# Performance work log

Measured on AMD Instinct MI355X. Metric: run time of the kernel, lower is better.

## Reference

```python
import jax, jax.numpy as jnp
import numpy as np

N_NODES = 100000
N_EDGES = 1600000
HIDDEN = 64
LEAKY_SLOPE = 0.01  # torch F.leaky_relu default


def setup_inputs() -> dict:
    key = jax.random.key(0)
    k1, k2, k3, k4 = jax.random.split(key, 4)
    x = jax.random.normal(k1, (N_NODES, HIDDEN), dtype=jnp.float32)
    edge_index = jax.random.randint(k2, (2, N_EDGES), 0, N_NODES, dtype=jnp.int64)
    # Linear(hidden, 1, bias=False) weights, squeezed to [hidden]
    w_i = jax.random.normal(k3, (HIDDEN,), dtype=jnp.float32) * 0.1
    w_j = jax.random.normal(k4, (HIDDEN,), dtype=jnp.float32) * 0.1
    return {"x": x, "edge_index": edge_index, "w_i": w_i, "w_j": w_j}


def reference(x, edge_index, w_i, w_j):
    n = x.shape[0]
    ej, ei = edge_index[0], edge_index[1]  # (edge_index_j, edge_index_i)
    # per-node attention scores, then per-edge gather
    s_i = x @ w_i  # [N]
    s_j = x @ w_j  # [N]
    e = jax.nn.leaky_relu(s_i[ei] + s_j[ej], LEAKY_SLOPE)  # [E]
    # segment softmax over edges grouped by destination node ei
    emax = jax.ops.segment_max(e, ei, num_segments=n)  # [N]
    ex = jnp.exp(e - emax[ei])  # [E]
    denom = jax.ops.segment_sum(ex, ei, num_segments=n)  # [N]
    alpha = ex / denom[ei]  # [E]
    # spmm: out[i] = sum_{edges e: dst=i} alpha_e * x[src_e]
    out = jax.ops.segment_sum(alpha[:, None] * x[ej], ei, num_segments=n)  # [N, H]
    return jax.nn.relu(out)
```

## Files before the change

kernel.cpp:

```cpp
#include <hip/hip_runtime.h>
#include <stdint.h>

#define N_NODES 100000
#define N_EDGES 1600000
#define HIDDEN  64
#define SLOPE   0.01f
#define NBUCK   782
#define CAPB    2816
#define PCHUNK  16384
#define NPART   98
#define NSB     391
#define NCAP    48


__device__ __forceinline__ unsigned short f2bf(float f) {
    uint32_t u = __float_as_uint(f);
    uint32_t r = u + 0x7FFFu + ((u >> 16) & 1u);
    return (unsigned short)(r >> 16);
}

__global__ void __launch_bounds__(1024) k_build(const float* __restrict__ x,
                                                const float* __restrict__ w_i,
                                                const float* __restrict__ w_j,
                                                const int* __restrict__ srcs,
                                                const int* __restrict__ dsts,
                                                float* __restrict__ s_i,
                                                float* __restrict__ s_j,
                                                unsigned short* __restrict__ xb,
                                                int* __restrict__ ctrl,
                                                uint32_t* __restrict__ pairs) {
    __shared__ int lcnt[NBUCK], lloc[NBUCK], lbase[NBUCK];
    __shared__ int scan[1024];
    __shared__ uint32_t srec[PCHUNK];
    int tid = threadIdx.x;
    if (blockIdx.x < NPART) {
        if (blockIdx.x == 0) {
            if (tid < NBUCK) atomicExch(&ctrl[tid], 0);
            __syncthreads();
            if (tid == 0) { __threadfence(); atomicExch(&ctrl[NBUCK], 1); }
        }
        if (tid < NBUCK) lcnt[tid] = 0;
        __syncthreads();
        int e0 = blockIdx.x * PCHUNK;
        int e1 = min(e0 + PCHUNK, N_EDGES);
        for (int e = e0 + tid; e < e1; e += 1024)
            atomicAdd(&lcnt[dsts[e] >> 7], 1);
        __syncthreads();
        int v = (tid < NBUCK) ? lcnt[tid] : 0;
        scan[tid] = v;
        __syncthreads();
        for (int off = 1; off < 1024; off <<= 1) {
            int t = (tid >= off) ? scan[tid - off] : 0;
            __syncthreads();
            scan[tid] += t;
            __syncthreads();
        }
        if (tid < NBUCK) lloc[tid] = scan[tid] - v;
        if (tid == 0)
            while (atomicAdd(&ctrl[NBUCK], 0) != 1) {}
        __syncthreads();
        if (tid < NBUCK) {
            lbase[tid] = v ? atomicAdd(&ctrl[tid], v) : 0;
            lcnt[tid] = 0;
        }
        __syncthreads();
        for (int e = e0 + tid; e < e1; e += 1024) {
            int src = srcs[e];
            int dst = dsts[e];
            int b = dst >> 7;
            int r = atomicAdd(&lcnt[b], 1);
            srec[lloc[b] + r] = ((uint32_t)(dst & 127) << 24) | (uint32_t)src;
        }
        __syncthreads();
        int wv = tid >> 6, ln = tid & 63;
        for (int b = wv; b < NBUCK; b += 16) {
            int c = lcnt[b];
            int lo = lloc[b], go = lbase[b];
            for (int j = ln; j < c; j += 64) {
                int pos = go + j;
                if (pos < CAPB)
                    pairs[(size_t)b * CAPB + pos] = srec[lo + j];
            }
        }
        return;
    }
    int u0 = blockIdx.x - NPART;
    int g16 = tid >> 4;
    int ql = tid & 15;
    float4 wi4 = ((const float4*)w_i)[ql];
    float4 wj4 = ((const float4*)w_j)[ql];
#pragma unroll
    for (int i = 0; i < 4; ++i) {
        int node = u0 * 256 + i * 64 + g16;
        if (node >= N_NODES) break;
        float4 v = ((const float4*)x)[node * 16 + ql];
        float a = v.x * wi4.x + v.y * wi4.y + v.z * wi4.z + v.w * wi4.w;
        float b = v.x * wj4.x + v.y * wj4.y + v.z * wj4.z + v.w * wj4.w;
#pragma unroll
        for (int off = 1; off < 16; off <<= 1) {
            a += __shfl_xor(a, off, 64);
            b += __shfl_xor(b, off, 64);
        }
        if (ql == 0) { s_i[node] = a; s_j[node] = b; }
        ushort4 o;
        o.x = f2bf(v.x); o.y = f2bf(v.y); o.z = f2bf(v.z); o.w = f2bf(v.w);
        ((ushort4*)xb)[node * 16 + ql] = o;
    }
}

__device__ __forceinline__ float bflo(uint32_t d) { return __uint_as_float(d << 16); }
__device__ __forceinline__ float bfhi(uint32_t d) { return __uint_as_float(d & 0xFFFF0000u); }

template <int L>
__device__ __forceinline__ void gat_batch4(const uint64_t* pp, int i, int quarter, int ql,
                                           const uint2* __restrict__ xw2,
                                           float acc[4], float& den) {
    uint64_t q[L];
    uint2 d[L];
#pragma unroll
    for (int t = 0; t < L; ++t) q[t] = pp[i + 4 * t + quarter];
#pragma unroll
    for (int t = 0; t < L; ++t)
        d[t] = xw2[((uint32_t)q[t] & 0xFFFFFFu) * 16 + ql];
#pragma unroll
    for (int t = 0; t < L; ++t) {
        float w = __uint_as_float((uint32_t)(q[t] >> 32));
        den += w;
        acc[0] = fmaf(w, bflo(d[t].x), acc[0]);
        acc[1] = fmaf(w, bfhi(d[t].x), acc[1]);
        acc[2] = fmaf(w, bflo(d[t].y), acc[2]);
        acc[3] = fmaf(w, bfhi(d[t].y), acc[3]);
    }
}

__global__ void __launch_bounds__(1024, 8) k_bucket_agg(const uint2* __restrict__ xw2,
                                                        const uint32_t* __restrict__ pairs,
                                                        const int* __restrict__ ctrl,
                                                        const float* __restrict__ s_i,
                                                        const float* __restrict__ s_j,
                                                        float* __restrict__ out) {
    __shared__ uint64_t spairs[128 * NCAP];
    __shared__ int lcur[128];
    __shared__ float s_si[128];
    int tid = threadIdx.x;
    int cb = blockIdx.x;
    int node0 = cb * 128;
    const uint32_t* reg = pairs + (size_t)cb * CAPB;
    int rcnt = min(ctrl[cb], CAPB);
    if (tid < 128) {
        lcur[tid] = 0;
        int node = node0 + tid;
        s_si[tid] = (node < N_NODES) ? s_i[node] : 0.f;
    }
    __syncthreads();
    for (int e = tid; e < rcnt; e += 1024) {
        uint32_t p = reg[e];
        int n = (int)(p >> 24);
        int src = (int)(p & 0xFFFFFFu);
        float sc = s_si[n] + s_j[src];
        sc = (sc > 0.f) ? sc : SLOPE * sc;
        float w = __expf(sc);
        int slot = atomicAdd(&lcur[n], 1);
        if (slot < NCAP)
            spairs[n * NCAP + slot] =
                ((uint64_t)__float_as_uint(w) << 32) | (uint32_t)src;
    }
    __syncthreads();
    int wave = tid >> 6, lane = tid & 63;
    int quarter = lane >> 4, ql = lane & 15;
    for (int k = wave; k < 128; k += 16) {
        int node = node0 + k;
        if (node >= N_NODES) break;
        float acc[4] = {0.f, 0.f, 0.f, 0.f};
        float den = 0.f;
        int c = lcur[k];
        if (c <= NCAP) {
            const uint64_t* pp = spairs + k * NCAP;
            int i = 0;
            for (; i + 16 <= c; i += 16) gat_batch4<4>(pp, i, quarter, ql, xw2, acc, den);
            if (i + 8 <= c) { gat_batch4<2>(pp, i, quarter, ql, xw2, acc, den); i += 8; }
            if (i + 4 <= c) { gat_batch4<1>(pp, i, quarter, ql, xw2, acc, den); i += 4; }
            int rem = c - i;
            if (rem > 0) {
                uint64_t q = pp[i + min(quarter, rem - 1)];
                float w = (quarter < rem) ? __uint_as_float((uint32_t)(q >> 32)) : 0.f;
                uint2 d = xw2[((uint32_t)q & 0xFFFFFFu) * 16 + ql];
                den += w;
                acc[0] = fmaf(w, bflo(d.x), acc[0]);
                acc[1] = fmaf(w, bfhi(d.x), acc[1]);
                acc[2] = fmaf(w, bflo(d.y), acc[2]);
                acc[3] = fmaf(w, bfhi(d.y), acc[3]);
            }
        } else {
            for (int e = 0; e < rcnt; ++e) {
                uint32_t p = reg[e];
                if ((int)(p >> 24) == k) {
                    int src = (int)(p & 0xFFFFFFu);
                    float sc = s_si[k] + s_j[src];
                    sc = (sc > 0.f) ? sc : SLOPE * sc;
                    float w = (quarter == 0) ? __expf(sc) : 0.f;
                    uint2 d = xw2[(uint32_t)src * 16 + ql];
                    den += w;
                    acc[0] = fmaf(w, bflo(d.x), acc[0]);
                    acc[1] = fmaf(w, bfhi(d.x), acc[1]);
                    acc[2] = fmaf(w, bflo(d.y), acc[2]);
                    acc[3] = fmaf(w, bfhi(d.y), acc[3]);
                }
            }
        }
#pragma unroll
        for (int j = 0; j < 4; ++j) {
            acc[j] += __shfl_xor(acc[j], 16, 64);
            acc[j] += __shfl_xor(acc[j], 32, 64);
        }
        den += __shfl_xor(den, 16, 64);
        den += __shfl_xor(den, 32, 64);
        if (quarter == 0) {
            float4 r = make_float4(0.f, 0.f, 0.f, 0.f);
            if (c > 0) {
                float inv = 1.f / den;
                r.x = fmaxf(acc[0] * inv, 0.f);
                r.y = fmaxf(acc[1] * inv, 0.f);
                r.z = fmaxf(acc[2] * inv, 0.f);
                r.w = fmaxf(acc[3] * inv, 0.f);
            }
            ((float4*)(out + (size_t)node * HIDDEN))[ql] = r;
        }
    }
}

extern "C" void kernel_launch(void* const* d_in, const int* in_sizes, int n_in,
                              void* d_out, int out_size, void* d_ws, size_t ws_size,
                              hipStream_t stream) {
    const float* x   = (const float*)d_in[0];
    const int*   ei  = (const int*)d_in[1];
    const float* w_i = (const float*)d_in[2];
    const float* w_j = (const float*)d_in[3];
    float* out = (float*)d_out;

    char* p = (char*)d_ws;
    float*          s_i   = (float*)p;          p += (size_t)N_NODES * 4;
    float*          s_j   = (float*)p;          p += (size_t)N_NODES * 4;
    unsigned short* xb    = (unsigned short*)p; p += (size_t)N_NODES * HIDDEN * 2;
    int*            ctrl  = (int*)p;            p += 4096;
    uint32_t*       pairs = (uint32_t*)p;

    const int* srcs = ei;
    const int* dsts = ei + N_EDGES;

    k_build     <<<NPART + NSB, 1024, 0, stream>>>(x, w_i, w_j, srcs, dsts,
                                                   s_i, s_j, xb, ctrl, pairs);
    k_bucket_agg<<<NBUCK, 1024, 0, stream>>>((const uint2*)xb, pairs, ctrl,
                                             s_i, s_j, out);
}
```

Baseline: 151.6 us.

## Assign one node per quarter-wave instead of splitting edges across quarters

The aggregation loop now gives each 16-lane quarter of a wave its own destination node, so a wave processes four nodes at once. Each quarter walks its node's edge list with predicated 4-wide loads up to the wave maximum, which removes the cross-quarter shuffle reduction. NCAP goes from 48 to 49, changing the shared-memory row stride and presumably spreading LDS bank use. The cost is load imbalance inside a wave when neighbour counts differ, plus wasted masked loads of row 0.

```diff
diff --git a/kernel.cpp b/kernel.cpp
--- a/kernel.cpp
+++ b/kernel.cpp
@@ -10,7 +10,7 @@
 #define PCHUNK  16384
 #define NPART   98
 #define NSB     391
-#define NCAP    48
+#define NCAP    49
 
 
 __device__ __forceinline__ unsigned short f2bf(float f) {
@@ -111,28 +111,6 @@
 __device__ __forceinline__ float bflo(uint32_t d) { return __uint_as_float(d << 16); }
 __device__ __forceinline__ float bfhi(uint32_t d) { return __uint_as_float(d & 0xFFFF0000u); }
 
-template <int L>
-__device__ __forceinline__ void gat_batch4(const uint64_t* pp, int i, int quarter, int ql,
-                                           const uint2* __restrict__ xw2,
-                                           float acc[4], float& den) {
-    uint64_t q[L];
-    uint2 d[L];
-#pragma unroll
-    for (int t = 0; t < L; ++t) q[t] = pp[i + 4 * t + quarter];
-#pragma unroll
-    for (int t = 0; t < L; ++t)
-        d[t] = xw2[((uint32_t)q[t] & 0xFFFFFFu) * 16 + ql];
-#pragma unroll
-    for (int t = 0; t < L; ++t) {
-        float w = __uint_as_float((uint32_t)(q[t] >> 32));
-        den += w;
-        acc[0] = fmaf(w, bflo(d[t].x), acc[0]);
-        acc[1] = fmaf(w, bfhi(d[t].x), acc[1]);
-        acc[2] = fmaf(w, bflo(d[t].y), acc[2]);
-        acc[3] = fmaf(w, bfhi(d[t].y), acc[3]);
-    }
-}
-
 __global__ void __launch_bounds__(1024, 8) k_bucket_agg(const uint2* __restrict__ xw2,
                                                         const uint32_t* __restrict__ pairs,
                                                         const int* __restrict__ ctrl,
@@ -168,61 +146,68 @@
     __syncthreads();
     int wave = tid >> 6, lane = tid & 63;
     int quarter = lane >> 4, ql = lane & 15;
-    for (int k = wave; k < 128; k += 16) {
+    for (int half = 0; half < 2; ++half) {
+        int k = wave * 4 + quarter + 64 * half;
         int node = node0 + k;
-        if (node >= N_NODES) break;
-        float acc[4] = {0.f, 0.f, 0.f, 0.f};
-        float den = 0.f;
-        int c = lcur[k];
-        if (c <= NCAP) {
-            const uint64_t* pp = spairs + k * NCAP;
-            int i = 0;
-            for (; i + 16 <= c; i += 16) gat_batch4<4>(pp, i, quarter, ql, xw2, acc, den);
-            if (i + 8 <= c) { gat_batch4<2>(pp, i, quarter, ql, xw2, acc, den); i += 8; }
-            if (i + 4 <= c) { gat_batch4<1>(pp, i, quarter, ql, xw2, acc, den); i += 4; }
-            int rem = c - i;
-            if (rem > 0) {
-                uint64_t q = pp[i + min(quarter, rem - 1)];
-                float w = (quarter < rem) ? __uint_as_float((uint32_t)(q >> 32)) : 0.f;
-                uint2 d = xw2[((uint32_t)q & 0xFFFFFFu) * 16 + ql];
+        int creal = lcur[k];
+        int cq = min(creal, NCAP);
+        int mx = cq;
+        mx = max(mx, __shfl_xor(mx, 16, 64));
+        mx = max(mx, __shfl_xor(mx, 32, 64));
+        const uint64_t* pp = spairs + k * NCAP;
+        float acc0 = 0.f, acc1 = 0.f, acc2 = 0.f, acc3 = 0.f, den = 0.f;
+        for (int j = 0; j < mx; j += 4) {
+            uint64_t qv[4];
+#pragma unroll
+            for (int u = 0; u < 4; ++u) {
+                int idx = j + u;
+                qv[u] = pp[(idx < cq) ? idx : 0];
+            }
+            uint2 d[4];
+            float wv[4];
+#pragma unroll
+            for (int u = 0; u < 4; ++u) {
+                int idx = j + u;
+                uint32_t src = (idx < cq) ? ((uint32_t)qv[u] & 0xFFFFFFu) : 0u;
+                wv[u] = (idx < cq) ? __uint_as_float((uint32_t)(qv[u] >> 32)) : 0.f;
+                d[u] = xw2[src * 16 + ql];
+            }
+#pragma unroll
+            for (int u = 0; u < 4; ++u) {
+                float w = wv[u];
                 den += w;
-                acc[0] = fmaf(w, bflo(d.x), acc[0]);
-                acc[1] = fmaf(w, bfhi(d.x), acc[1]);
-                acc[2] = fmaf(w, bflo(d.y), acc[2]);
-                acc[3] = fmaf(w, bfhi(d.y), acc[3]);
-            }
-        } else {
+                acc0 = fmaf(w, bflo(d[u].x), acc0);
+                acc1 = fmaf(w, bfhi(d[u].x), acc1);
+                acc2 = fmaf(w, bflo(d[u].y), acc2);
+                acc3 = fmaf(w, bfhi(d[u].y), acc3);
+            }
+        }
+        if (creal > NCAP) {
+            acc0 = acc1 = acc2 = acc3 = 0.f; den = 0.f;
             for (int e = 0; e < rcnt; ++e) {
                 uint32_t p = reg[e];
                 if ((int)(p >> 24) == k) {
                     int src = (int)(p & 0xFFFFFFu);
                     float sc = s_si[k] + s_j[src];
                     sc = (sc > 0.f) ? sc : SLOPE * sc;
-                    float w = (quarter == 0) ? __expf(sc) : 0.f;
-                    uint2 d = xw2[(uint32_t)src * 16 + ql];
+                    float w = __expf(sc);
+                    uint2 dd = xw2[(uint32_t)src * 16 + ql];
                     den += w;
-                    acc[0] = fmaf(w, bflo(d.x), acc[0]);
-                    acc[1] = fmaf(w, bfhi(d.x), acc[1]);
-                    acc[2] = fmaf(w, bflo(d.y), acc[2]);
-                    acc[3] = fmaf(w, bfhi(d.y), acc[3]);
+                    acc0 = fmaf(w, bflo(dd.x), acc0);
+                    acc1 = fmaf(w, bfhi(dd.x), acc1);
+                    acc2 = fmaf(w, bflo(dd.y), acc2);
+                    acc3 = fmaf(w, bfhi(dd.y), acc3);
                 }
             }
         }
-#pragma unroll
-        for (int j = 0; j < 4; ++j) {
-            acc[j] += __shfl_xor(acc[j], 16, 64);
-            acc[j] += __shfl_xor(acc[j], 32, 64);
-        }
-        den += __shfl_xor(den, 16, 64);
-        den += __shfl_xor(den, 32, 64);
-        if (quarter == 0) {
+        if (node < N_NODES) {
             float4 r = make_float4(0.f, 0.f, 0.f, 0.f);
-            if (c > 0) {
+            if (creal > 0) {
                 float inv = 1.f / den;
-                r.x = fmaxf(acc[0] * inv, 0.f);
-                r.y = fmaxf(acc[1] * inv, 0.f);
-                r.z = fmaxf(acc[2] * inv, 0.f);
-                r.w = fmaxf(acc[3] * inv, 0.f);
+                r.x = fmaxf(acc0 * inv, 0.f);
+                r.y = fmaxf(acc1 * inv, 0.f);
+                r.z = fmaxf(acc2 * inv, 0.f);
+                r.w = fmaxf(acc3 * inv, 0.f);
             }
             ((float4*)(out + (size_t)node * HIDDEN))[ql] = r;
         }
```

Result: faster. 145.3 us (-4.2%).
